# Optimization experiments

Hardware: AMD Instinct MI355X
Metric: run time of the kernel (lower is better)

The kernel has to match this reference:

```python
import jax, jax.numpy as jnp
import numpy as np

N, D, H, E, TOPK = 4096, 512, 2048, 8, 2


def setup_inputs() -> dict:
    key = jax.random.key(0)
    k0, k1, k2, k3 = jax.random.split(key, 4)
    scale = 0.02
    return {
        "inp": jax.random.normal(k0, (N, D), jnp.float32),
        "gate_w": jax.random.normal(k1, (D, E), jnp.float32) * scale,
        "gate_b": jnp.zeros((E,), jnp.float32),
        "w1": jax.random.normal(k2, (E, D, H), jnp.float32) * scale,
        "b1": jnp.zeros((E, H), jnp.float32),
        "w2": jax.random.normal(k3, (E, H, D), jnp.float32) * scale,
        "b2": jnp.zeros((E, D), jnp.float32),
        "top_k": TOPK,
    }


def reference(inp, gate_w, gate_b, w1, b1, w2, b2, top_k):
    # --- NaiveGate: linear -> top-k -> softmax over the k selected logits ---
    logits = inp @ gate_w + gate_b                      # [N, E]
    topk_val, topk_idx = jax.lax.top_k(logits, top_k)   # [N, k]
    gate_score = jax.nn.softmax(topk_val, axis=-1)       # [N, k]

    n_tok = inp.shape[0]
    n_exp = gate_w.shape[1]

    # Combine weight per (token, expert): sum of gate scores of slots routed
    # to that expert. Mathematically identical to FastMoE's
    # repeat_interleave -> scatter -> expert_fn -> gather -> bmm(gate_score, x).
    combine = jnp.zeros((n_tok, n_exp), inp.dtype)
    combine = combine.at[jnp.arange(n_tok)[:, None], topk_idx].add(gate_score)

    # --- Experts: 2-layer FFN (d_model -> 4*d_model -> d_model) with GELU ---
    out = jnp.zeros_like(inp)
    for e in range(n_exp):  # small fixed expert count
        h = jax.nn.gelu(inp @ w1[e] + b1[e])             # [N, H]
        y = h @ w2[e] + b2[e]                            # [N, D]
        out = out + combine[:, e:e + 1] * y
    return out
```

## Files before the change

kernel.cpp:

```cpp
#include <hip/hip_runtime.h>
#include <hip/hip_bf16.h>
#include <stdint.h>

#define NTOK 4096
#define DM   512
#define HD   2048
#define NE   8

typedef __bf16 bf16x8 __attribute__((ext_vector_type(8)));
typedef float  f32x4  __attribute__((ext_vector_type(4)));

__device__ __forceinline__ unsigned short f2bf(float f) {
  unsigned int u = __float_as_uint(f);
  u += 0x7FFF + ((u >> 16) & 1);
  return (unsigned short)(u >> 16);
}

__device__ __forceinline__ float gelu_fast(float x) {
  float s = 1.5957691216f * (x + 0.044715f * x * x * x);
  return x / (1.f + __expf(-s));
}

__device__ __forceinline__ void gload_lds16(const void* g, void* l) {
  __builtin_amdgcn_global_load_lds(
      (__attribute__((address_space(1))) const void*)g,
      (__attribute__((address_space(3))) void*)l,
      16, 0, 0);
}

template<int K, int N>
__device__ __forceinline__ void transw_dev(
    const float* __restrict__ in, unsigned short* __restrict__ out,
    int bid, int t, float (*tile)[33]) {
  const int tpe = (K / 32) * (N / 32);
  int e   = bid / tpe;
  int rem = bid % tpe;
  int kt  = rem / (N / 32), nt = rem % (N / 32);
  int tx  = t & 31, ty = t >> 5;
  const float* src = in + ((size_t)e * K + kt * 32) * N + (size_t)nt * 32;
  #pragma unroll
  for (int i = 0; i < 4; i++) {
    int r = ty + i * 8;
    tile[r][tx] = src[(size_t)r * N + tx];
  }
  __syncthreads();
  unsigned short* dst = out + ((size_t)e * N + nt * 32) * K + (size_t)kt * 32;
  #pragma unroll
  for (int i = 0; i < 4; i++) {
    int rr = ty + i * 8;
    dst[(size_t)rr * K + tx] = f2bf(tile[tx][rr]);
  }
}

__global__ __launch_bounds__(256) void prep_kernel(
    const float* __restrict__ inp, const float* __restrict__ w1,
    const float* __restrict__ w2, const float* __restrict__ gw,
    const float* __restrict__ gb, unsigned short* __restrict__ Xb,
    unsigned short* __restrict__ W1T, unsigned short* __restrict__ W2T,
    int* __restrict__ eidx, float* __restrict__ wgtA) {
  __shared__ float tile[32][33];
  const int b = blockIdx.x;
  const int t = threadIdx.x;

  if (b < 1024) {
    int i = b * 256 + t;
    const f32x4* p = (const f32x4*)(inp + (size_t)i * 8);
    f32x4 v0 = p[0], v1 = p[1];
    union { unsigned short s[8]; uint4 u; } o;
    #pragma unroll
    for (int j = 0; j < 4; j++) { o.s[j] = f2bf(v0[j]); o.s[4 + j] = f2bf(v1[j]); }
    *(uint4*)(Xb + (size_t)i * 8) = o.u;
  } else if (b < 9216) {
    transw_dev<DM, HD>(w1, W1T, b - 1024, t, tile);
  } else if (b < 17408) {
    transw_dev<HD, DM>(w2, W2T, b - 9216, t, tile);
  } else {
    int tok = (b - 17408) * 4 + (t >> 6);
    int l   = t & 63;
    const float* x = inp + (size_t)tok * DM;
    float acc[NE];
    #pragma unroll
    for (int e = 0; e < NE; e++) acc[e] = 0.f;
    #pragma unroll
    for (int j = 0; j < DM / 64; j++) {
      int d = j * 64 + l;
      float xv = x[d];
      const float* g = gw + (size_t)d * NE;
      #pragma unroll
      for (int e = 0; e < NE; e++) acc[e] += xv * g[e];
    }
    #pragma unroll
    for (int off = 32; off >= 1; off >>= 1) {
      #pragma unroll
      for (int e = 0; e < NE; e++) acc[e] += __shfl_xor(acc[e], off, 64);
    }
    if (l == 0) {
      float lg[NE];
      #pragma unroll
      for (int e = 0; e < NE; e++) lg[e] = acc[e] + gb[e];
      int i0 = 0;
      #pragma unroll
      for (int e = 1; e < NE; e++) if (lg[e] > lg[i0]) i0 = e;
      int i1 = (i0 == 0) ? 1 : 0;
      #pragma unroll
      for (int e = 0; e < NE; e++) if (e != i0 && lg[e] > lg[i1]) i1 = e;
      float ev = expf(lg[i1] - lg[i0]);
      float w0 = 1.f / (1.f + ev);
      float w1s = ev * w0;
      wgtA[tok * 2]     = w0;
      wgtA[tok * 2 + 1] = w1s;
      eidx[tok * 2]     = i0;
      eidx[tok * 2 + 1] = i1;
    }
  }
}

__global__ __launch_bounds__(256) void build_lists(
    const int* __restrict__ eidx, int* __restrict__ lists,
    int* __restrict__ counts) {
  __shared__ int wsums[4];
  __shared__ int base;
  const int e = blockIdx.x;
  const int t = threadIdx.x;
  const int lane = t & 63, w = t >> 6;
  if (t == 0) base = 0;
  __syncthreads();
  for (int it = 0; it < 2 * NTOK / 256; ++it) {
    int i = it * 256 + t;
    int match = (eidx[i] == e) ? 1 : 0;
    unsigned long long b = __ballot(match);
    int wsum = __popcll(b);
    int lpre = __popcll(b & ((1ull << lane) - 1ull));
    if (lane == 0) wsums[w] = wsum;
    __syncthreads();
    int wpre = 0;
    #pragma unroll
    for (int k = 0; k < 4; k++) if (k < w) wpre += wsums[k];
    int tot = wsums[0] + wsums[1] + wsums[2] + wsums[3];
    if (match) lists[e * NTOK + base + wpre + lpre] = i;
    __syncthreads();
    if (t == 0) base += tot;
    __syncthreads();
  }
  if (t == 0) counts[e] = base;
}

template<int KDIM, int NDIM, bool IS_L1>
__global__ __launch_bounds__(256) void moe_gemm(
    const unsigned short* __restrict__ A,
    const unsigned short* __restrict__ WT,
    const float* __restrict__ bias,
    const int* __restrict__ lists,
    const int* __restrict__ counts,
    unsigned short* __restrict__ Hout) {
  __shared__ unsigned short ldsA[128 * 128];
  __shared__ unsigned short ldsB[128 * 128];
  __shared__ int ldsE[128];

  const int CT  = NDIM / 128;
  const int e   = blockIdx.x & 7;
  const int idx = blockIdx.x >> 3;
  const int rt  = idx / CT;
  const int ct  = idx % CT;
  const int cnt = counts[e];
  if (rt * 128 >= cnt) return;

  const int t = threadIdx.x;
  if (t < 128) {
    int rg = rt * 128 + t;
    ldsE[t] = lists[e * NTOK + (rg < cnt ? rg : cnt - 1)];
  }
  __syncthreads();

  const int lane = t & 63;
  const int wid  = t >> 6;
  const int wr = wid >> 1, wc = wid & 1;
  const int rowsel = t >> 4;
  const int chunk  = (t & 15) ^ (rowsel & 7);

  const unsigned short* aptr[8];
  const unsigned short* bptr[8];
  #pragma unroll
  for (int i = 0; i < 8; i++) {
    int rl = i * 16 + rowsel;
    int entry = ldsE[rl];
    long arow = IS_L1 ? (entry >> 1) : entry;
    aptr[i] = A + arow * (long)KDIM + chunk * 8;
    bptr[i] = WT + ((long)e * NDIM + ct * 128 + rl) * KDIM + chunk * 8;
  }

  f32x4 acc[4][4] = {};

  const int NKT = KDIM / 128;
  for (int kt = 0; kt < NKT; ++kt) {
    #pragma unroll
    for (int i = 0; i < 8; i++) {
      gload_lds16(aptr[i] + kt * 128, (char*)ldsA + i * 4096 + wid * 1024);
      gload_lds16(bptr[i] + kt * 128, (char*)ldsB + i * 4096 + wid * 1024);
    }
    __syncthreads();
    #pragma unroll
    for (int kk = 0; kk < 4; ++kk) {
      bf16x8 a[4], b[4];
      int ko = kk * 32 + (lane >> 4) * 8;
      #pragma unroll
      for (int m = 0; m < 4; m++) {
        int ra = wr * 64 + m * 16 + (lane & 15);
        a[m] = *(const bf16x8*)&ldsA[ra * 128 + (ko ^ ((ra & 7) << 3))];
      }
      #pragma unroll
      for (int n = 0; n < 4; n++) {
        int rb = wc * 64 + n * 16 + (lane & 15);
        b[n] = *(const bf16x8*)&ldsB[rb * 128 + (ko ^ ((rb & 7) << 3))];
      }
      #pragma unroll
      for (int m = 0; m < 4; m++)
        #pragma unroll
        for (int n = 0; n < 4; n++)
          acc[m][n] = __builtin_amdgcn_mfma_f32_16x16x32_bf16(a[m], b[n], acc[m][n], 0, 0, 0);
    }
    __syncthreads();
  }

  {
    float bv[4];
    #pragma unroll
    for (int n = 0; n < 4; n++)
      bv[n] = IS_L1 ? bias[e * NDIM + ct * 128 + wc * 64 + n * 16 + (lane & 15)] : 0.f;
    #pragma unroll
    for (int m = 0; m < 4; m++) {
      int rbase = wr * 64 + m * 16 + (lane >> 4) * 4;
      #pragma unroll
      for (int n = 0; n < 4; n++) {
        int col = wc * 64 + n * 16 + (lane & 15);
        #pragma unroll
        for (int r = 0; r < 4; r++) {
          float v = acc[m][n][r] + bv[n];
          ldsB[(rbase + r) * 128 + col] = f2bf(IS_L1 ? gelu_fast(v) : v);
        }
      }
    }
  }
  __syncthreads();

  #pragma unroll
  for (int it = 0; it < 8; ++it) {
    int row = it * 16 + (t >> 4);
    if (rt * 128 + row >= cnt) continue;
    int ent = ldsE[row];
    int ch  = t & 15;
    uint4 v = *(const uint4*)&ldsB[row * 128 + ch * 8];
    *(uint4*)(Hout + (size_t)ent * NDIM + ct * 128 + ch * 8) = v;
  }
}

__global__ __launch_bounds__(256) void combine_kernel(
    const unsigned short* __restrict__ Y,
    const float* __restrict__ b2,
    const int* __restrict__ eidx,
    const float* __restrict__ wgtA,
    float* __restrict__ out) {
  const int t   = threadIdx.x;
  const int tok = blockIdx.x * 4 + (t >> 6);
  const int c0  = (t & 63) * 8;
  const int e0 = eidx[tok * 2], e1 = eidx[tok * 2 + 1];
  const float w0 = wgtA[tok * 2], w1 = wgtA[tok * 2 + 1];
  uint4 y0 = *(const uint4*)(Y + (size_t)(tok * 2) * DM + c0);
  uint4 y1 = *(const uint4*)(Y + (size_t)(tok * 2 + 1) * DM + c0);
  const unsigned short* y0s = (const unsigned short*)&y0;
  const unsigned short* y1s = (const unsigned short*)&y1;
  const float* bb0 = b2 + (size_t)e0 * DM + c0;
  const float* bb1 = b2 + (size_t)e1 * DM + c0;
  float o[8];
  #pragma unroll
  for (int j = 0; j < 8; j++) {
    float v0 = __uint_as_float((unsigned)y0s[j] << 16);
    float v1 = __uint_as_float((unsigned)y1s[j] << 16);
    o[j] = w0 * (v0 + bb0[j]) + w1 * (v1 + bb1[j]);
  }
  *(f32x4*)(out + (size_t)tok * DM + c0)     = *(f32x4*)&o[0];
  *(f32x4*)(out + (size_t)tok * DM + c0 + 4) = *(f32x4*)&o[4];
}

extern "C" void kernel_launch(void* const* d_in, const int* in_sizes, int n_in,
                              void* d_out, int out_size, void* d_ws, size_t ws_size,
                              hipStream_t stream) {
  const float* inp = (const float*)d_in[0];
  const float* gw  = (const float*)d_in[1];
  const float* gb  = (const float*)d_in[2];
  const float* w1  = (const float*)d_in[3];
  const float* b1  = (const float*)d_in[4];
  const float* w2  = (const float*)d_in[5];
  const float* b2  = (const float*)d_in[6];
  float* out = (float*)d_out;

  char* ws = (char*)d_ws;
  unsigned short* Xb   = (unsigned short*)(ws + 0);
  unsigned short* W1T  = (unsigned short*)(ws + 4194304);
  unsigned short* W2T  = (unsigned short*)(ws + 20971520);
  unsigned short* Hbuf = (unsigned short*)(ws + 37748736);
  int*   lists  = (int*)  (ws + 71303168);
  float* wgtA   = (float*)(ws + 71434240);
  int*   counts = (int*)  (ws + 71467008);
  int*   eidx   = (int*)  (ws + 71467072);
  unsigned short* Ybuf = (unsigned short*)(ws + 0);

  prep_kernel<<<18432, 256, 0, stream>>>(inp, w1, w2, gw, gb,
                                         Xb, W1T, W2T, eidx, wgtA);
  build_lists<<<NE, 256, 0, stream>>>(eidx, lists, counts);
  moe_gemm<DM, HD, true ><<<8 * 32 * (HD / 128), 256, 0, stream>>>(
      Xb, W1T, b1, lists, counts, Hbuf);
  moe_gemm<HD, DM, false><<<8 * 32 * (DM / 128), 256, 0, stream>>>(
      Hbuf, W2T, b2, lists, counts, Ybuf);
  combine_kernel<<<NTOK / 4, 256, 0, stream>>>(Ybuf, b2, eidx, wgtA, out);
}
```

Measured before the change: 122.6 us.

## Use 256x128 tiles with 512 threads and split-K for second expert GEMM

The grouped expert GEMM moves from 128x128 tiles with a 128-wide K step to 256-row tiles, a 64-wide K step and 512 threads, so each weight tile is reused across more tokens. The second-layer GEMM also splits K in two and writes two partial outputs into separate halves of the Y buffer. The combine kernel then adds both partials. This aims at better weight reuse and more blocks for the small-N second GEMM, at the cost of extra partial-output traffic, a two-pass epilogue through LDS, and grids that launch more empty blocks.

Measured after the change: 116.3 us, median of 2. 5.1% less time.

```diff
diff --git a/kernel.cpp b/kernel.cpp
--- a/kernel.cpp
+++ b/kernel.cpp
@@ -145,29 +145,31 @@
   if (t == 0) counts[e] = base;
 }
 
-template<int KDIM, int NDIM, bool IS_L1>
-__global__ __launch_bounds__(256) void moe_gemm(
+template<int KDIM, int NDIM, bool IS_L1, int KSPLIT>
+__global__ __launch_bounds__(512) void moe_gemm(
     const unsigned short* __restrict__ A,
     const unsigned short* __restrict__ WT,
     const float* __restrict__ bias,
     const int* __restrict__ lists,
     const int* __restrict__ counts,
     unsigned short* __restrict__ Hout) {
-  __shared__ unsigned short ldsA[128 * 128];
-  __shared__ unsigned short ldsB[128 * 128];
-  __shared__ int ldsE[128];
+  __shared__ unsigned short ldsA[256 * 64];
+  __shared__ unsigned short ldsB[128 * 64];
+  __shared__ int ldsE[256];
 
   const int CT  = NDIM / 128;
   const int e   = blockIdx.x & 7;
   const int idx = blockIdx.x >> 3;
-  const int rt  = idx / CT;
   const int ct  = idx % CT;
+  const int r1  = idx / CT;
+  const int ks  = r1 % KSPLIT;
+  const int rt  = r1 / KSPLIT;
   const int cnt = counts[e];
-  if (rt * 128 >= cnt) return;
+  if (rt * 256 >= cnt) return;
 
   const int t = threadIdx.x;
-  if (t < 128) {
-    int rg = rt * 128 + t;
+  if (t < 256) {
+    int rg = rt * 256 + t;
     ldsE[t] = lists[e * NTOK + (rg < cnt ? rg : cnt - 1)];
   }
   __syncthreads();
@@ -175,43 +177,49 @@
   const int lane = t & 63;
   const int wid  = t >> 6;
   const int wr = wid >> 1, wc = wid & 1;
-  const int rowsel = t >> 4;
-  const int chunk  = (t & 15) ^ (rowsel & 7);
-
-  const unsigned short* aptr[8];
-  const unsigned short* bptr[8];
-  #pragma unroll
-  for (int i = 0; i < 8; i++) {
-    int rl = i * 16 + rowsel;
+  const int rowsel = t >> 3;
+  const int colsel = (t & 7) ^ (rowsel & 7);
+
+  const int KCH = KDIM / KSPLIT;
+  const unsigned short* aptr[4];
+  #pragma unroll
+  for (int i = 0; i < 4; i++) {
+    int rl = i * 64 + rowsel;
     int entry = ldsE[rl];
     long arow = IS_L1 ? (entry >> 1) : entry;
-    aptr[i] = A + arow * (long)KDIM + chunk * 8;
-    bptr[i] = WT + ((long)e * NDIM + ct * 128 + rl) * KDIM + chunk * 8;
+    aptr[i] = A + arow * (long)KDIM + ks * KCH + colsel * 8;
+  }
+  const unsigned short* bptr[2];
+  #pragma unroll
+  for (int j = 0; j < 2; j++) {
+    int brow = ct * 128 + j * 64 + rowsel;
+    bptr[j] = WT + ((long)e * NDIM + brow) * KDIM + ks * KCH + colsel * 8;
   }
 
   f32x4 acc[4][4] = {};
-
-  const int NKT = KDIM / 128;
+  const int NKT = KCH / 64;
+
   for (int kt = 0; kt < NKT; ++kt) {
     #pragma unroll
-    for (int i = 0; i < 8; i++) {
-      gload_lds16(aptr[i] + kt * 128, (char*)ldsA + i * 4096 + wid * 1024);
-      gload_lds16(bptr[i] + kt * 128, (char*)ldsB + i * 4096 + wid * 1024);
-    }
-    __syncthreads();
-    #pragma unroll
-    for (int kk = 0; kk < 4; ++kk) {
+    for (int i = 0; i < 4; i++)
+      gload_lds16(aptr[i] + kt * 64, (char*)ldsA + i * 8192 + t * 16);
+    #pragma unroll
+    for (int j = 0; j < 2; j++)
+      gload_lds16(bptr[j] + kt * 64, (char*)ldsB + j * 8192 + t * 16);
+    __syncthreads();
+    #pragma unroll
+    for (int kk = 0; kk < 2; ++kk) {
       bf16x8 a[4], b[4];
       int ko = kk * 32 + (lane >> 4) * 8;
       #pragma unroll
       for (int m = 0; m < 4; m++) {
-        int ra = wr * 64 + m * 16 + (lane & 15);
-        a[m] = *(const bf16x8*)&ldsA[ra * 128 + (ko ^ ((ra & 7) << 3))];
+        int rx = wr * 64 + m * 16 + (lane & 15);
+        a[m] = *(const bf16x8*)&ldsA[rx * 64 + (ko ^ ((rx & 7) << 3))];
       }
       #pragma unroll
       for (int n = 0; n < 4; n++) {
-        int rb = wc * 64 + n * 16 + (lane & 15);
-        b[n] = *(const bf16x8*)&ldsB[rb * 128 + (ko ^ ((rb & 7) << 3))];
+        int rx = wc * 64 + n * 16 + (lane & 15);
+        b[n] = *(const bf16x8*)&ldsB[rx * 64 + (ko ^ ((rx & 7) << 3))];
       }
       #pragma unroll
       for (int m = 0; m < 4; m++)
@@ -222,35 +230,43 @@
     __syncthreads();
   }
 
-  {
-    float bv[4];
-    #pragma unroll
-    for (int n = 0; n < 4; n++)
-      bv[n] = IS_L1 ? bias[e * NDIM + ct * 128 + wc * 64 + n * 16 + (lane & 15)] : 0.f;
-    #pragma unroll
-    for (int m = 0; m < 4; m++) {
-      int rbase = wr * 64 + m * 16 + (lane >> 4) * 4;
-      #pragma unroll
-      for (int n = 0; n < 4; n++) {
-        int col = wc * 64 + n * 16 + (lane & 15);
+  float bv[4];
+  #pragma unroll
+  for (int n = 0; n < 4; n++)
+    bv[n] = IS_L1 ? bias[e * NDIM + ct * 128 + wc * 64 + n * 16 + (lane & 15)] : 0.f;
+  unsigned short* ldsO = ldsA;
+  unsigned short* Hbase = Hout + (size_t)ks * 8192 * NDIM;
+
+  #pragma unroll
+  for (int half = 0; half < 2; ++half) {
+    if ((wr >> 1) == half) {
+      #pragma unroll
+      for (int m = 0; m < 4; m++) {
+        int lrow = (wr & 1) * 64 + m * 16 + (lane >> 4) * 4;
         #pragma unroll
-        for (int r = 0; r < 4; r++) {
-          float v = acc[m][n][r] + bv[n];
-          ldsB[(rbase + r) * 128 + col] = f2bf(IS_L1 ? gelu_fast(v) : v);
+        for (int n = 0; n < 4; n++) {
+          int col = wc * 64 + n * 16 + (lane & 15);
+          #pragma unroll
+          for (int r = 0; r < 4; r++) {
+            float v = acc[m][n][r] + bv[n];
+            ldsO[(lrow + r) * 128 + col] = f2bf(IS_L1 ? gelu_fast(v) : v);
+          }
         }
       }
     }
-  }
-  __syncthreads();
-
-  #pragma unroll
-  for (int it = 0; it < 8; ++it) {
-    int row = it * 16 + (t >> 4);
-    if (rt * 128 + row >= cnt) continue;
-    int ent = ldsE[row];
-    int ch  = t & 15;
-    uint4 v = *(const uint4*)&ldsB[row * 128 + ch * 8];
-    *(uint4*)(Hout + (size_t)ent * NDIM + ct * 128 + ch * 8) = v;
+    __syncthreads();
+    #pragma unroll
+    for (int rnd = 0; rnd < 4; ++rnd) {
+      int lrow = rnd * 32 + (t >> 4);
+      int row  = half * 128 + lrow;
+      if (rt * 256 + row < cnt) {
+        int ent = ldsE[row];
+        int ch  = t & 15;
+        uint4 v = *(const uint4*)&ldsO[lrow * 128 + ch * 8];
+        *(uint4*)(Hbase + (size_t)ent * NDIM + ct * 128 + ch * 8) = v;
+      }
+    }
+    __syncthreads();
   }
 }
 
@@ -263,20 +279,23 @@
   const int t   = threadIdx.x;
   const int tok = blockIdx.x * 4 + (t >> 6);
   const int c0  = (t & 63) * 8;
-  const int e0 = eidx[tok * 2], e1 = eidx[tok * 2 + 1];
-  const float w0 = wgtA[tok * 2], w1 = wgtA[tok * 2 + 1];
-  uint4 y0 = *(const uint4*)(Y + (size_t)(tok * 2) * DM + c0);
-  uint4 y1 = *(const uint4*)(Y + (size_t)(tok * 2 + 1) * DM + c0);
-  const unsigned short* y0s = (const unsigned short*)&y0;
-  const unsigned short* y1s = (const unsigned short*)&y1;
-  const float* bb0 = b2 + (size_t)e0 * DM + c0;
-  const float* bb1 = b2 + (size_t)e1 * DM + c0;
-  float o[8];
-  #pragma unroll
-  for (int j = 0; j < 8; j++) {
-    float v0 = __uint_as_float((unsigned)y0s[j] << 16);
-    float v1 = __uint_as_float((unsigned)y1s[j] << 16);
-    o[j] = w0 * (v0 + bb0[j]) + w1 * (v1 + bb1[j]);
+  float o[8] = {};
+  #pragma unroll
+  for (int slot = 0; slot < 2; ++slot) {
+    int ent = tok * 2 + slot;
+    int es  = eidx[ent];
+    float ws = wgtA[ent];
+    uint4 y0 = *(const uint4*)(Y + (size_t)ent * DM + c0);
+    uint4 y1 = *(const uint4*)(Y + (size_t)(8192 + ent) * DM + c0);
+    const unsigned short* s0 = (const unsigned short*)&y0;
+    const unsigned short* s1 = (const unsigned short*)&y1;
+    const float* bb = b2 + (size_t)es * DM + c0;
+    #pragma unroll
+    for (int j = 0; j < 8; j++) {
+      float v = __uint_as_float((unsigned)s0[j] << 16)
+              + __uint_as_float((unsigned)s1[j] << 16);
+      o[j] += ws * (v + bb[j]);
+    }
   }
   *(f32x4*)(out + (size_t)tok * DM + c0)     = *(f32x4*)&o[0];
   *(f32x4*)(out + (size_t)tok * DM + c0 + 4) = *(f32x4*)&o[4];
@@ -308,9 +327,9 @@
   prep_kernel<<<18432, 256, 0, stream>>>(inp, w1, w2, gw, gb,
                                          Xb, W1T, W2T, eidx, wgtA);
   build_lists<<<NE, 256, 0, stream>>>(eidx, lists, counts);
-  moe_gemm<DM, HD, true ><<<8 * 32 * (HD / 128), 256, 0, stream>>>(
+  moe_gemm<DM, HD, true, 1><<<8 * 32 * (HD / 128), 512, 0, stream>>>(
       Xb, W1T, b1, lists, counts, Hbuf);
-  moe_gemm<HD, DM, false><<<8 * 32 * (DM / 128), 256, 0, stream>>>(
+  moe_gemm<HD, DM, false, 2><<<8 * 32 * 2 * (DM / 128), 512, 0, stream>>>(
       Hbuf, W2T, b2, lists, counts, Ybuf);
   combine_kernel<<<NTOK / 4, 256, 0, stream>>>(Ybuf, b2, eidx, wgtA, out);
 }
```
